# Kernel optimization log

Measured on AMD Instinct MI355X. Metric: run time of the kernel, lower is better.

Reference implementation:

```python
import jax, jax.numpy as jnp
import numpy as np


def setup_inputs() -> dict:
    key = jax.random.key(0)
    ks = jax.random.split(key, 6)
    B, H, N, BS, W, T, D = 1, 32, 256, 32, 128, 4096, 128
    q = jax.random.normal(ks[0], (B, H, N * BS, D), dtype=jnp.float32)
    k_ctx = jax.random.normal(ks[1], (B, H, T, D), dtype=jnp.float32)
    v_ctx = jax.random.normal(ks[2], (B, H, T, D), dtype=jnp.float32)
    k_draft = jax.random.normal(ks[3], (B, H, N * BS, D), dtype=jnp.float32)
    v_draft = jax.random.normal(ks[4], (B, H, N * BS, D), dtype=jnp.float32)
    anchor_positions = jnp.sort(
        jax.random.randint(ks[5], (B, N), 0, T - BS), axis=-1
    )
    block_keep_mask = jnp.ones((B, N), dtype=bool)
    return {
        "q": q, "k_ctx": k_ctx, "v_ctx": v_ctx,
        "k_draft": k_draft, "v_draft": v_draft,
        "anchor_positions": anchor_positions,
        "block_keep_mask": block_keep_mask,
        "context_window": 128,
    }


def reference(q, k_ctx, v_ctx, k_draft, v_draft,
              anchor_positions, block_keep_mask, context_window):
    # FlashMTP block-sparse attention (FlexAttention mask_mod semantics):
    #   query block i attends to context tokens t in [max(0, a_i - W), a_i - 1]
    #   plus its own draft block (bidirectional); invalid blocks see nothing.
    B, H, Q, D = q.shape
    N = anchor_positions.shape[1]
    bs = Q // N
    T = k_ctx.shape[2]
    W = context_window
    scale = 1.0 / np.sqrt(D).astype(np.float32)

    # sliding context window indices per block: (B, N, W)
    idx = anchor_positions[:, :, None] - W + jnp.arange(W)[None, None, :]
    valid_ctx = idx >= 0  # idx < anchor always holds by construction
    idxc = jnp.clip(idx, 0, T - 1)
    gidx = idxc.reshape(B, 1, N * W, 1)
    k_win = jnp.take_along_axis(k_ctx, gidx, axis=2).reshape(B, H, N, W, D)
    v_win = jnp.take_along_axis(v_ctx, gidx, axis=2).reshape(B, H, N, W, D)

    qb = q.reshape(B, H, N, bs, D)
    kb = k_draft.reshape(B, H, N, bs, D)
    vb = v_draft.reshape(B, H, N, bs, D)

    s_ctx = jnp.einsum('bhnqd,bhnwd->bhnqw', qb, k_win) * scale
    s_blk = jnp.einsum('bhnqd,bhnkd->bhnqk', qb, kb) * scale

    keep = block_keep_mask[:, None, :, None, None]           # (B,1,N,1,1)
    m_ctx = valid_ctx[:, None, :, None, :] & keep            # (B,1,N,1,W)
    m_blk = jnp.broadcast_to(keep, (B, 1, N, 1, bs))         # (B,1,N,1,bs)
    mask = jnp.concatenate([m_ctx, m_blk], axis=-1)
    s = jnp.concatenate([s_ctx, s_blk], axis=-1)
    neg = jnp.asarray(-1e30, s.dtype)
    p = jax.nn.softmax(jnp.where(mask, s, neg), axis=-1)

    v_all = jnp.concatenate([v_win, vb], axis=3)             # (B,H,N,W+bs,D)
    out = jnp.einsum('bhnqk,bhnkd->bhnqd', p, v_all)
    out = out * keep.astype(out.dtype)  # invalid blocks -> zero output
    return out.reshape(B, H, Q, D)
```

## Files before the change

kernel.cpp:

```cpp
#include <hip/hip_runtime.h>

constexpr int H_  = 32;
constexpr int N_  = 256;
constexpr int BS_ = 32;
constexpr int W_  = 128;
constexpr int T_  = 4096;
constexpr int D_  = 128;
constexpr int NQ_ = 8192;
constexpr float SCALE_  = 0.08838834764831845f;
constexpr float L2E_    = 1.4426950408889634f;
constexpr float MFLOOR_ = -1.0e28f;
constexpr float DEFER_  = 8.0f;

typedef __attribute__((ext_vector_type(4))) float f4;
typedef __attribute__((ext_vector_type(4))) short s4;
typedef __attribute__((ext_vector_type(8))) short s8;
typedef __attribute__((ext_vector_type(4))) float fx4;
typedef __attribute__((ext_vector_type(2))) int i2;

__device__ __forceinline__ int pack2(float a, float b) {
  int r;
  asm("v_cvt_pk_bf16_f32 %0, %1, %2" : "=v"(r) : "v"(a), "v"(b));
  return r;
}

union frag_u { int w[4]; s8 v; };

__device__ __forceinline__ void lds_barrier() {
  asm volatile("s_waitcnt lgkmcnt(0)" ::: "memory");
  __builtin_amdgcn_s_barrier();
}

__global__ __launch_bounds__(128, 2)
void mtp_attn_kernel(const float* __restrict__ q,
                     const float* __restrict__ k_ctx,
                     const float* __restrict__ v_ctx,
                     const float* __restrict__ k_draft,
                     const float* __restrict__ v_draft,
                     const int* __restrict__ anchor,
                     const int* __restrict__ keepm,
                     float* __restrict__ out)
{
  int u = blockIdx.x;
  u = (u & 7) * 1024 + (u >> 3);
  const int h = u >> 8;
  const int n = u & 255;

  const int tu   = threadIdx.x;
  const int lane = tu & 63;
  const int wu   = tu >> 6;
  const int l15  = lane & 15;
  const int g    = lane >> 4;
  const int rb   = tu >> 5;
  const int c4   = tu & 31;

  const int A  = anchor[n];
  const int kp = keepm[n];
  const int wm = W_ - A;

  __shared__ __align__(16) unsigned char smem_[35328];
  short* Kb[2] = { (short*)smem_,          (short*)(smem_ + 8448) };
  short* Vb[2] = { (short*)(smem_ + 16896), (short*)(smem_ + 16896 + 9216) };

  const float* qrow = q + ((size_t)h * NQ_ + (size_t)n * BS_ + wu * 16 + l15) * D_;
  s8 qb[4];
#pragma unroll
  for (int ks = 0; ks < 4; ++ks) {
    f4 f0 = *reinterpret_cast<const f4*>(qrow + ks * 32 + g * 4);
    f4 f1 = *reinterpret_cast<const f4*>(qrow + ks * 32 + 16 + g * 4);
    frag_u uq;
    uq.w[0] = pack2(f0[0], f0[1]); uq.w[1] = pack2(f0[2], f0[3]);
    uq.w[2] = pack2(f1[0], f1[1]); uq.w[3] = pack2(f1[2], f1[3]);
    qb[ks] = uq.v;
  }

  const float* kcb = k_ctx + (size_t)h * T_ * D_;
  const float* vcb = v_ctx + (size_t)h * T_ * D_;
  const float* kdb = k_draft + ((size_t)h * NQ_ + (size_t)n * BS_) * D_;
  const float* vdb = v_draft + ((size_t)h * NQ_ + (size_t)n * BS_) * D_;

  f4 krA[8], vrA[8], krB[8], vrB[8];

  auto loadK = [&](f4 (&dst)[8], int c) {
    if (c < 4) {
      int base = (A - W_ + c * 32) * 32;
      const f4* kc4 = reinterpret_cast<const f4*>(kcb);
#pragma unroll
      for (int i = 0; i < 8; ++i) {
        int off = base + tu + 128 * i;
        off = off < 0 ? 0 : off;
        dst[i] = kc4[off];
      }
    } else {
      const f4* kd4 = reinterpret_cast<const f4*>(kdb);
#pragma unroll
      for (int i = 0; i < 8; ++i) dst[i] = kd4[tu + 128 * i];
    }
  };
  auto loadV = [&](f4 (&dst)[8], int c) {
#pragma unroll
    for (int p = 0; p < 2; ++p)
#pragma unroll
      for (int i = 0; i < 4; ++i) {
        int row = p * 16 + rb * 4 + i;
        const float* src;
        if (c < 4) { int idx = A - W_ + c * 32 + row; idx = idx < 0 ? 0 : idx; src = vcb + (size_t)idx * D_; }
        else       { src = vdb + (size_t)row * D_; }
        dst[p * 4 + i] = reinterpret_cast<const f4*>(src)[c4];
      }
  };
  auto writeK = [&](f4 (&src)[8], short* kb) {
#pragma unroll
    for (int i = 0; i < 8; ++i) {
      int row = (tu >> 5) + 4 * i;
      i2 w = { pack2(src[i][0], src[i][1]), pack2(src[i][2], src[i][3]) };
      *reinterpret_cast<i2*>(kb + row * 132 + c4 * 4) = w;
    }
  };
  auto writeV = [&](f4 (&src)[8], short* vT) {
#pragma unroll
    for (int p = 0; p < 2; ++p) {
      int keyl = p * 16 + rb * 4;
#pragma unroll
      for (int j = 0; j < 4; ++j) {
        i2 w = { pack2(src[p * 4 + 0][j], src[p * 4 + 1][j]),
                 pack2(src[p * 4 + 2][j], src[p * 4 + 3][j]) };
        *reinterpret_cast<i2*>(vT + (c4 * 4 + j) * 36 + keyl) = w;
      }
    }
  };

  loadK(krA, 0); loadV(vrA, 0);
  loadK(krB, 1); loadV(vrB, 1);
  writeK(krA, Kb[0]); writeV(vrA, Vb[0]);
  loadK(krA, 2); loadV(vrA, 2);

  float m  = -3.0e38f;
  float ls = 0.0f;
  fx4 oacc[8];
#pragma unroll
  for (int t = 0; t < 8; ++t) oacc[t] = {0.f, 0.f, 0.f, 0.f};

  lds_barrier();

#pragma unroll
  for (int c = 0; c < 5; ++c) {
    if (c < 4) {
      f4 (&kw)[8] = ((c + 1) & 1) ? krB : krA;
      f4 (&vw)[8] = ((c + 1) & 1) ? vrB : vrA;
      writeK(kw, Kb[(c + 1) & 1]);
      writeV(vw, Vb[(c + 1) & 1]);
      if (c < 3) { loadK(kw, c + 3); loadV(vw, c + 3); }
    }

    const short* kb = Kb[c & 1];
    fx4 st[2] = { {0.f,0.f,0.f,0.f}, {0.f,0.f,0.f,0.f} };
    __builtin_amdgcn_s_setprio(1);
#pragma unroll
    for (int ks = 0; ks < 4; ++ks) {
#pragma unroll
      for (int t2 = 0; t2 < 2; ++t2) {
        const short* kpr = kb + (t2 * 16 + l15) * 132 + ks * 32 + g * 4;
        s4 b0 = *reinterpret_cast<const s4*>(kpr);
        s4 b1 = *reinterpret_cast<const s4*>(kpr + 16);
        s8 kf = { b0[0], b0[1], b0[2], b0[3], b1[0], b1[1], b1[2], b1[3] };
        st[t2] = __builtin_amdgcn_mfma_f32_16x16x32_bf16(kf, qb[ks], st[t2], 0, 0, 0);
      }
    }
    __builtin_amdgcn_s_setprio(0);

    float sv[2][4];
    float cm = -3.0e38f;
#pragma unroll
    for (int t2 = 0; t2 < 2; ++t2) {
      int kb0 = c * 32 + t2 * 16 + g * 4;
#pragma unroll
      for (int r = 0; r < 4; ++r) {
        float v = st[t2][r] * SCALE_;
        bool valid = (c == 4) || (kb0 + r >= wm);
        v = valid ? v : -1.0e30f;
        sv[t2][r] = v;
        cm = fmaxf(cm, v);
      }
    }
    cm = fmaxf(cm, __shfl_xor(cm, 16));
    cm = fmaxf(cm, __shfl_xor(cm, 32));

    if (c == 0) {
      m = fmaxf(cm, MFLOOR_);
    } else {
      float pm = fmaxf(m, cm);
      if (!__all(pm - m <= DEFER_)) {
        float mn = fmaxf(pm, MFLOOR_);
        float al = exp2f((m - mn) * L2E_);
        ls *= al;
        float alr[4];
#pragma unroll
        for (int r = 0; r < 4; ++r) alr[r] = __shfl(al, g * 4 + r);
#pragma unroll
        for (int nt = 0; nt < 8; ++nt)
#pragma unroll
          for (int r = 0; r < 4; ++r) oacc[nt][r] *= alr[r];
        m = mn;
      }
    }

    float pv[8];
#pragma unroll
    for (int t2 = 0; t2 < 2; ++t2)
#pragma unroll
      for (int r = 0; r < 4; ++r) {
        float p = exp2f((sv[t2][r] - m) * L2E_);
        ls += p;
        pv[t2 * 4 + r] = p;
      }
    frag_u up;
    up.w[0] = pack2(pv[0], pv[1]); up.w[1] = pack2(pv[2], pv[3]);
    up.w[2] = pack2(pv[4], pv[5]); up.w[3] = pack2(pv[6], pv[7]);
    s8 pa = up.v;

    const short* vT = Vb[c & 1];
    __builtin_amdgcn_s_setprio(1);
#pragma unroll
    for (int nt = 0; nt < 8; ++nt) {
      const short* vp = vT + (nt * 16 + l15) * 36 + g * 4;
      s4 b0 = *reinterpret_cast<const s4*>(vp);
      s4 b1 = *reinterpret_cast<const s4*>(vp + 16);
      s8 vb2 = { b0[0], b0[1], b0[2], b0[3], b1[0], b1[1], b1[2], b1[3] };
      oacc[nt] = __builtin_amdgcn_mfma_f32_16x16x32_bf16(pa, vb2, oacc[nt], 0, 0, 0);
    }
    __builtin_amdgcn_s_setprio(0);

    if (c < 4) lds_barrier();
  }

  ls += __shfl_xor(ls, 16);
  ls += __shfl_xor(ls, 32);
  float linv[4];
#pragma unroll
  for (int r = 0; r < 4; ++r) {
    float lq = __shfl(ls, g * 4 + r);
    linv[r] = kp ? (1.0f / lq) : 0.0f;
  }
  float* ob = out + ((size_t)h * NQ_ + (size_t)n * BS_ + wu * 16 + g * 4) * D_ + l15;
#pragma unroll
  for (int nt = 0; nt < 8; ++nt)
#pragma unroll
    for (int r = 0; r < 4; ++r)
      ob[(size_t)r * D_ + nt * 16] = oacc[nt][r] * linv[r];
}

extern "C" void kernel_launch(void* const* d_in, const int* in_sizes, int n_in,
                              void* d_out, int out_size, void* d_ws, size_t ws_size,
                              hipStream_t stream) {
  (void)in_sizes; (void)n_in; (void)d_ws; (void)ws_size; (void)out_size;
  const float* q       = (const float*)d_in[0];
  const float* k_ctx   = (const float*)d_in[1];
  const float* v_ctx   = (const float*)d_in[2];
  const float* k_draft = (const float*)d_in[3];
  const float* v_draft = (const float*)d_in[4];
  const int*   anchor  = (const int*)d_in[5];
  const int*   keep    = (const int*)d_in[6];
  float*       out     = (float*)d_out;
  mtp_attn_kernel<<<dim3(8192), dim3(128), 0, stream>>>(
      q, k_ctx, v_ctx, k_draft, v_draft, anchor, keep, out);
}
```

Baseline: 152.6 us.

## Software-pipeline QK^T into previous iteration and prefetch V fragments early

Moves the QK^T MFMA for the next chunk to right after the barrier at the end of each iteration, and loads all V fragments from LDS at the start of each iteration, before the global loads and LDS writes for the next chunk. The goal is to overlap LDS latency and MFMA work with the softmax and staging work. It also skips the cross-lane max reductions in the common case where the lane-local max stays within the deferral threshold. The cost is higher register pressure from 16 extra s4 V fragments held live, which could hurt occupancy under the launch bounds of 128 threads and 2 blocks.

```diff
diff --git a/kernel.cpp b/kernel.cpp
--- a/kernel.cpp
+++ b/kernel.cpp
@@ -59,7 +59,7 @@
   const int wm = W_ - A;
 
   __shared__ __align__(16) unsigned char smem_[35328];
-  short* Kb[2] = { (short*)smem_,          (short*)(smem_ + 8448) };
+  short* Kb[2] = { (short*)smem_,           (short*)(smem_ + 8448) };
   short* Vb[2] = { (short*)(smem_ + 16896), (short*)(smem_ + 16896 + 9216) };
 
   const float* qrow = q + ((size_t)h * NQ_ + (size_t)n * BS_ + wu * 16 + l15) * D_;
@@ -141,10 +141,39 @@
 #pragma unroll
   for (int t = 0; t < 8; ++t) oacc[t] = {0.f, 0.f, 0.f, 0.f};
 
+  fx4 st[2];
+
+  auto qk = [&](int cc) {
+    const short* kb = Kb[cc & 1];
+    st[0] = {0.f,0.f,0.f,0.f}; st[1] = {0.f,0.f,0.f,0.f};
+    __builtin_amdgcn_s_setprio(1);
+#pragma unroll
+    for (int ks = 0; ks < 4; ++ks)
+#pragma unroll
+      for (int t2 = 0; t2 < 2; ++t2) {
+        const short* kpr = kb + (t2 * 16 + l15) * 132 + ks * 32 + g * 4;
+        s4 b0 = *reinterpret_cast<const s4*>(kpr);
+        s4 b1 = *reinterpret_cast<const s4*>(kpr + 16);
+        s8 kf = { b0[0], b0[1], b0[2], b0[3], b1[0], b1[1], b1[2], b1[3] };
+        st[t2] = __builtin_amdgcn_mfma_f32_16x16x32_bf16(kf, qb[ks], st[t2], 0, 0, 0);
+      }
+    __builtin_amdgcn_s_setprio(0);
+  };
+
   lds_barrier();
+  qk(0);
 
 #pragma unroll
   for (int c = 0; c < 5; ++c) {
+    const short* vT = Vb[c & 1];
+    s4 vf0[8], vf1[8];
+#pragma unroll
+    for (int nt = 0; nt < 8; ++nt) {
+      const short* vp = vT + (nt * 16 + l15) * 36 + g * 4;
+      vf0[nt] = *reinterpret_cast<const s4*>(vp);
+      vf1[nt] = *reinterpret_cast<const s4*>(vp + 16);
+    }
+
     if (c < 4) {
       f4 (&kw)[8] = ((c + 1) & 1) ? krB : krA;
       f4 (&vw)[8] = ((c + 1) & 1) ? vrB : vrA;
@@ -153,24 +182,8 @@
       if (c < 3) { loadK(kw, c + 3); loadV(vw, c + 3); }
     }
 
-    const short* kb = Kb[c & 1];
-    fx4 st[2] = { {0.f,0.f,0.f,0.f}, {0.f,0.f,0.f,0.f} };
-    __builtin_amdgcn_s_setprio(1);
-#pragma unroll
-    for (int ks = 0; ks < 4; ++ks) {
-#pragma unroll
-      for (int t2 = 0; t2 < 2; ++t2) {
-        const short* kpr = kb + (t2 * 16 + l15) * 132 + ks * 32 + g * 4;
-        s4 b0 = *reinterpret_cast<const s4*>(kpr);
-        s4 b1 = *reinterpret_cast<const s4*>(kpr + 16);
-        s8 kf = { b0[0], b0[1], b0[2], b0[3], b1[0], b1[1], b1[2], b1[3] };
-        st[t2] = __builtin_amdgcn_mfma_f32_16x16x32_bf16(kf, qb[ks], st[t2], 0, 0, 0);
-      }
-    }
-    __builtin_amdgcn_s_setprio(0);
-
     float sv[2][4];
-    float cm = -3.0e38f;
+    float cmx = -3.0e38f;
 #pragma unroll
     for (int t2 = 0; t2 < 2; ++t2) {
       int kb0 = c * 32 + t2 * 16 + g * 4;
@@ -180,29 +193,27 @@
         bool valid = (c == 4) || (kb0 + r >= wm);
         v = valid ? v : -1.0e30f;
         sv[t2][r] = v;
-        cm = fmaxf(cm, v);
-      }
-    }
-    cm = fmaxf(cm, __shfl_xor(cm, 16));
-    cm = fmaxf(cm, __shfl_xor(cm, 32));
-
+        cmx = fmaxf(cmx, v);
+      }
+    }
     if (c == 0) {
+      float cm = fmaxf(cmx, __shfl_xor(cmx, 16));
+      cm = fmaxf(cm, __shfl_xor(cm, 32));
       m = fmaxf(cm, MFLOOR_);
-    } else {
-      float pm = fmaxf(m, cm);
-      if (!__all(pm - m <= DEFER_)) {
-        float mn = fmaxf(pm, MFLOOR_);
-        float al = exp2f((m - mn) * L2E_);
-        ls *= al;
-        float alr[4];
-#pragma unroll
-        for (int r = 0; r < 4; ++r) alr[r] = __shfl(al, g * 4 + r);
-#pragma unroll
-        for (int nt = 0; nt < 8; ++nt)
-#pragma unroll
-          for (int r = 0; r < 4; ++r) oacc[nt][r] *= alr[r];
-        m = mn;
-      }
+    } else if (!__all(cmx - m <= DEFER_)) {
+      float cm = fmaxf(cmx, __shfl_xor(cmx, 16));
+      cm = fmaxf(cm, __shfl_xor(cm, 32));
+      float mn = fmaxf(fmaxf(m, cm), MFLOOR_);
+      float al = exp2f((m - mn) * L2E_);
+      ls *= al;
+      float alr[4];
+#pragma unroll
+      for (int r = 0; r < 4; ++r) alr[r] = __shfl(al, g * 4 + r);
+#pragma unroll
+      for (int nt = 0; nt < 8; ++nt)
+#pragma unroll
+        for (int r = 0; r < 4; ++r) oacc[nt][r] *= alr[r];
+      m = mn;
     }
 
     float pv[8];
@@ -219,19 +230,19 @@
     up.w[2] = pack2(pv[4], pv[5]); up.w[3] = pack2(pv[6], pv[7]);
     s8 pa = up.v;
 
-    const short* vT = Vb[c & 1];
     __builtin_amdgcn_s_setprio(1);
 #pragma unroll
     for (int nt = 0; nt < 8; ++nt) {
-      const short* vp = vT + (nt * 16 + l15) * 36 + g * 4;
-      s4 b0 = *reinterpret_cast<const s4*>(vp);
-      s4 b1 = *reinterpret_cast<const s4*>(vp + 16);
-      s8 vb2 = { b0[0], b0[1], b0[2], b0[3], b1[0], b1[1], b1[2], b1[3] };
+      s8 vb2 = { vf0[nt][0], vf0[nt][1], vf0[nt][2], vf0[nt][3],
+                 vf1[nt][0], vf1[nt][1], vf1[nt][2], vf1[nt][3] };
       oacc[nt] = __builtin_amdgcn_mfma_f32_16x16x32_bf16(pa, vb2, oacc[nt], 0, 0, 0);
     }
     __builtin_amdgcn_s_setprio(0);
 
-    if (c < 4) lds_barrier();
+    if (c < 4) {
+      lds_barrier();
+      qk(c + 1);
+    }
   }
 
   ls += __shfl_xor(ls, 16);
```

Measured after the change: 159.8 us. +4.7%, slower.
